# Performance work log

Hardware: AMD Instinct MI355X
Metric: run time of the kernel (lower is better)

## Reference

```python
import math
import jax, jax.numpy as jnp
import numpy as np

B, S, D, H, DH = 2, 2048, 2048, 16, 128  # batch, seq (= n_ctx), d_model, n_heads, d_head


def _alibi_slopes(n):
    def pow2(m):
        start = 2 ** (-2 ** (-(math.log2(m) - 3)))
        return [start * start ** i for i in range(m)]
    if math.log2(n).is_integer():
        return pow2(n)
    c = 2 ** math.floor(math.log2(n))
    return pow2(c) + _alibi_slopes(2 * c)[0::2][: n - c]


def _alibi_mask(n_heads, q_len, kv_len):
    # faithful to _gen_alibi_mask: causal -inf upper triangle + slope * key_position
    slopes = jnp.asarray(np.array(_alibi_slopes(n_heads), dtype=np.float32))  # [H]
    bias = slopes[:, None, None] * jnp.arange(kv_len, dtype=jnp.float32)[None, None, :]  # [H,1,kv]
    i = jnp.arange(q_len)[:, None]
    j = jnp.arange(kv_len)[None, :]
    causal = jnp.where(j > i, -jnp.inf, 0.0).astype(jnp.float32)  # [q,kv] (q_len == kv_len here)
    return causal[None, :, :] + bias  # [H,q,kv]


def setup_inputs() -> dict:
    key = jax.random.key(0)
    k1, k2, k3, k4, k5 = jax.random.split(key, 5)
    scale = 1.0 / math.sqrt(D)
    return {
        "resid_pre": jax.random.normal(k1, (B, S, D), dtype=jnp.float32),
        "Wq": jax.random.normal(k2, (H * DH, D), dtype=jnp.float32) * scale,
        "Wk": jax.random.normal(k3, (H * DH, D), dtype=jnp.float32) * scale,
        "Wv": jax.random.normal(k4, (H * DH, D), dtype=jnp.float32) * scale,
        "Wo": jax.random.normal(k5, (D, H * DH), dtype=jnp.float32) * scale,
    }


def reference(resid_pre, Wq, Wk, Wv, Wo):
    b, s, d = resid_pre.shape
    # nn.Linear(no bias): y = x @ W^T ; view to [b, s, H, DH]
    q = (resid_pre @ Wq.T).reshape(b, s, H, DH)
    k = (resid_pre @ Wk.T).reshape(b, s, H, DH)
    v = (resid_pre @ Wv.T).reshape(b, s, H, DH)
    # QK^T / sqrt(d_head), clamp, add ALiBi+causal mask
    scores = jnp.einsum('bqhd,bkhd->bhqk', q, k) / math.sqrt(DH)
    scores = jnp.clip(scores, -1024.0, 1024.0)
    scores = scores + _alibi_mask(H, s, s)[None]  # broadcast over batch
    attn = jax.nn.softmax(scores.astype(jnp.float32), axis=-1).astype(q.dtype)
    z = jnp.einsum('bhqk,bkhd->bqhd', attn, v)  # [b,s,H,DH]
    # out_proj.weight [D, H*DH] reshaped to [D, H, DH]; per-head out summed over heads
    out = jnp.einsum('bqhd,ohd->bqo', z, Wo.reshape(d, H, DH))
    return out
```

## Files before the change

### kernel.cpp

```cpp
#include <hip/hip_runtime.h>
#include <hip/hip_bf16.h>

typedef __attribute__((ext_vector_type(4))) float f32x4;
typedef __attribute__((ext_vector_type(8))) short bf16x8;
typedef __attribute__((ext_vector_type(4))) short short4v;

__device__ __forceinline__ short f2bf(float f) {
  union { float f; unsigned u; } x; x.f = f;
  unsigned r = x.u + 0x7fffu + ((x.u >> 16) & 1u);
  return (short)(r >> 16);
}

__device__ __forceinline__ float fexp2(float x) {
#if __has_builtin(__builtin_amdgcn_exp2f)
  return __builtin_amdgcn_exp2f(x);
#else
  return exp2f(x);
#endif
}

#define WAITVM(n) { asm volatile("s_waitcnt vmcnt(" #n ")" ::: "memory"); __builtin_amdgcn_sched_barrier(0); }
#define BARRIER() { __builtin_amdgcn_sched_barrier(0); asm volatile("s_barrier" ::: "memory"); __builtin_amdgcn_sched_barrier(0); }
#define GLD16(g, l) __builtin_amdgcn_global_load_lds((const __attribute__((address_space(1))) void*)(g), (__attribute__((address_space(3))) void*)(l), 16, 0, 0)

#define QSC (0.08838834764831845f * 1.4426950408889634f)

__global__ __launch_bounds__(256) void cast_kernel(const float* __restrict__ in,
                                                   short* __restrict__ out, int n4) {
  int i = blockIdx.x * 256 + threadIdx.x;
  if (i < n4) {
    const float4 v = reinterpret_cast<const float4*>(in)[i];
    short4v s;
    s.x = f2bf(v.x); s.y = f2bf(v.y); s.z = f2bf(v.z); s.w = f2bf(v.w);
    reinterpret_cast<short4v*>(out)[i] = s;
  }
}

__global__ __launch_bounds__(256) void cast_w_kernel(const float* __restrict__ w0,
                                                     const float* __restrict__ w1,
                                                     const float* __restrict__ w2,
                                                     const float* __restrict__ w3,
                                                     short* __restrict__ qkv,
                                                     short* __restrict__ wo) {
  const int y = blockIdx.y;
  const float* in = (y == 0) ? w0 : (y == 1) ? w1 : (y == 2) ? w2 : w3;
  short* out = (y < 3) ? (qkv + (long)y * 4194304) : wo;
  const int i = blockIdx.x * 256 + threadIdx.x;
  const float4 v = reinterpret_cast<const float4*>(in)[i];
  short4v s;
  s.x = f2bf(v.x); s.y = f2bf(v.y); s.z = f2bf(v.z); s.w = f2bf(v.w);
  reinterpret_cast<short4v*>(out)[i] = s;
}

__global__ __launch_bounds__(512, 2) void gemm_qkv8(const short* __restrict__ A,
                                                    const short* __restrict__ W,
                                                    short* __restrict__ Qo,
                                                    short* __restrict__ Ko,
                                                    short* __restrict__ Vt) {
  __shared__ __align__(1024) char lds[131072];
  const int tid  = threadIdx.x;
  const int lane = tid & 63;
  const int w    = tid >> 6;
  const int wm   = w >> 2, wn = w & 3;
  const int l16  = lane & 15, g = lane >> 4;
  const int K    = 2048;

  int id = (int)blockIdx.x;
  id = (id & 7) * 64 + (id >> 3);
  const int mb = id & 31, nb = id >> 5;
  const long m0 = (long)mb * 128, n0 = (long)nb * 384;

  const int srow = lane >> 3;
  const int scol = ((lane & 7) ^ srow) * 8;
  const int csw  = (l16 & 7) << 4;

  f32x4 acc[4][6];
  #pragma unroll
  for (int a = 0; a < 4; a++)
    #pragma unroll
    for (int b = 0; b < 6; b++) acc[a][b] = (f32x4){0.f, 0.f, 0.f, 0.f};

  #define STAGE_A(kt, buf)                                                          \
    {                                                                               \
      const short* s0_ = A + (m0 + w * 16 + srow) * K + (kt) * 64 + scol;           \
      char* d_ = lds + (buf) * 65536 + (w * 16) * 128;                              \
      GLD16(s0_, d_);                                                               \
      GLD16(s0_ + 8LL * K, d_ + 1024);                                              \
    }
  #define STAGE_B(h, kt, buf)                                                       \
    {                                                                               \
      const short* s0_ = W + (n0 + (h) * 128 + w * 16 + srow) * K + (kt) * 64 + scol; \
      char* d_ = lds + (buf) * 65536 + 16384 + (h) * 16384 + (w * 16) * 128;        \
      GLD16(s0_, d_);                                                               \
      GLD16(s0_ + 8LL * K, d_ + 1024);                                              \
    }

  #define RDA(buf, fmL, k) (*reinterpret_cast<const bf16x8*>(                       \
      lds + (buf) * 65536 + ((wm * 64 + (fmL) * 16 + l16) * 128) +                  \
      ((((k) * 64 + g * 16)) ^ csw)))
  #define RDB(buf, h, j, k) (*reinterpret_cast<const bf16x8*>(                      \
      lds + (buf) * 65536 + 16384 + (h) * 16384 +                                   \
      ((wn * 16 + (j) * 64 + l16) * 128) + ((((k) * 64 + g * 16)) ^ csw)))

  STAGE_A(0, 0);
  STAGE_B(0, 0, 0);
  STAGE_B(1, 0, 0);
  STAGE_B(2, 0, 0);
  WAITVM(4);
  BARRIER();

  bf16x8 af[4][2], bfr[2][2];
  for (int kt = 0; kt < 32; ++kt) {
    const int cur = kt & 1, nxt = cur ^ 1;
    const int ks = (kt + 1 < 32) ? (kt + 1) : kt;

    #pragma unroll
    for (int fm = 0; fm < 4; fm++)
      #pragma unroll
      for (int k = 0; k < 2; k++) af[fm][k] = RDA(cur, fm, k);
    #pragma unroll
    for (int j = 0; j < 2; j++)
      #pragma unroll
      for (int k = 0; k < 2; k++) bfr[j][k] = RDB(cur, 0, j, k);
    STAGE_A(ks, nxt);
    STAGE_B(0, ks, nxt);
    WAITVM(6);
    BARRIER();
    __builtin_amdgcn_s_setprio(1);
    #pragma unroll
    for (int fm = 0; fm < 4; fm++)
      #pragma unroll
      for (int j = 0; j < 2; j++)
        #pragma unroll
        for (int k = 0; k < 2; k++)
          acc[fm][j] = __builtin_amdgcn_mfma_f32_16x16x32_bf16(af[fm][k], bfr[j][k], acc[fm][j], 0, 0, 0);
    __builtin_amdgcn_s_setprio(0);
    BARRIER();

    #pragma unroll
    for (int j = 0; j < 2; j++)
      #pragma unroll
      for (int k = 0; k < 2; k++) bfr[j][k] = RDB(cur, 1, j, k);
    STAGE_B(1, ks, nxt);
    WAITVM(6);
    BARRIER();
    __builtin_amdgcn_s_setprio(1);
    #pragma unroll
    for (int fm = 0; fm < 4; fm++)
      #pragma unroll
      for (int j = 0; j < 2; j++)
        #pragma unroll
        for (int k = 0; k < 2; k++)
          acc[fm][2 + j] = __builtin_amdgcn_mfma_f32_16x16x32_bf16(af[fm][k], bfr[j][k], acc[fm][2 + j], 0, 0, 0);
    __builtin_amdgcn_s_setprio(0);
    BARRIER();

    #pragma unroll
    for (int j = 0; j < 2; j++)
      #pragma unroll
      for (int k = 0; k < 2; k++) bfr[j][k] = RDB(cur, 2, j, k);
    STAGE_B(2, ks, nxt);
    WAITVM(4);
    BARRIER();
    __builtin_amdgcn_s_setprio(1);
    #pragma unroll
    for (int fm = 0; fm < 4; fm++)
      #pragma unroll
      for (int j = 0; j < 2; j++)
        #pragma unroll
        for (int k = 0; k < 2; k++)
          acc[fm][4 + j] = __builtin_amdgcn_mfma_f32_16x16x32_bf16(af[fm][k], bfr[j][k], acc[fm][4 + j], 0, 0, 0);
    __builtin_amdgcn_s_setprio(0);
    BARRIER();
  }

  #pragma unroll
  for (int fm = 0; fm < 4; fm++)
    #pragma unroll
    for (int fj = 0; fj < 6; fj++) {
      const long row0 = m0 + wm * 64 + fm * 16 + g * 4;
      const long col  = n0 + fj * 64 + wn * 16 + l16;
      if (col < 2048) {
        #pragma unroll
        for (int i = 0; i < 4; i++) Qo[(row0 + i) * 2048 + col] = f2bf(acc[fm][fj][i] * QSC);
      } else if (col < 4096) {
        #pragma unroll
        for (int i = 0; i < 4; i++) Ko[(row0 + i) * 2048 + (col - 2048)] = f2bf(acc[fm][fj][i]);
      } else {
        const long c2 = col - 4096;
        const long base = (((row0 >> 11) * 16 + (c2 >> 7)) * 128 + (c2 & 127)) * 2048 + (row0 & 2047);
        short4v pk;
        #pragma unroll
        for (int i = 0; i < 4; i++) pk[i] = f2bf(acc[fm][fj][i]);
        *reinterpret_cast<short4v*>(Vt + base) = pk;
      }
    }
  #undef STAGE_A
  #undef STAGE_B
  #undef RDA
  #undef RDB
}

__global__ __launch_bounds__(512, 2) void gemm_o2(const short* __restrict__ A,
                                                  const short* __restrict__ W,
                                                  float* __restrict__ C) {
  __shared__ __align__(1024) char lds[98304];
  const int tid  = threadIdx.x;
  const int lane = tid & 63;
  const int w    = tid >> 6;
  const int wm   = w >> 2, wn = w & 3;
  const int l16  = lane & 15, g = lane >> 4;
  const int K    = 2048;

  int id = (int)blockIdx.x;
  id = (id & 7) * 32 + (id >> 3);
  const int mb = id & 31, nb = id >> 5;
  const long m0 = (long)mb * 128, n0 = (long)nb * 256;

  const int srow = lane >> 3;
  const int scol = ((lane & 7) ^ srow) * 8;
  const int csw  = (l16 & 7) << 4;

  f32x4 acc[4][4];
  #pragma unroll
  for (int a = 0; a < 4; a++)
    #pragma unroll
    for (int b = 0; b < 4; b++) acc[a][b] = (f32x4){0.f, 0.f, 0.f, 0.f};

  #define OSTAGE_A(kt, buf)                                                         \
    {                                                                               \
      const short* s0_ = A + (m0 + w * 16 + srow) * K + (kt) * 64 + scol;           \
      char* d_ = lds + (buf) * 49152 + (w * 16) * 128;                              \
      GLD16(s0_, d_);                                                               \
      GLD16(s0_ + 8LL * K, d_ + 1024);                                              \
    }
  #define OSTAGE_B(h, kt, buf)                                                      \
    {                                                                               \
      const short* s0_ = W + (n0 + (h) * 128 + w * 16 + srow) * K + (kt) * 64 + scol; \
      char* d_ = lds + (buf) * 49152 + 16384 + (h) * 16384 + (w * 16) * 128;        \
      GLD16(s0_, d_);                                                               \
      GLD16(s0_ + 8LL * K, d_ + 1024);                                              \
    }
  #define ORDA(buf, fmL, k) (*reinterpret_cast<const bf16x8*>(                      \
      lds + (buf) * 49152 + ((wm * 64 + (fmL) * 16 + l16) * 128) +                  \
      ((((k) * 64 + g * 16)) ^ csw)))
  #define ORDB(buf, h, j, k) (*reinterpret_cast<const bf16x8*>(                     \
      lds + (buf) * 49152 + 16384 + (h) * 16384 +                                   \
      ((wn * 16 + (j) * 64 + l16) * 128) + ((((k) * 64 + g * 16)) ^ csw)))

  OSTAGE_A(0, 0);
  OSTAGE_B(0, 0, 0);
  OSTAGE_B(1, 0, 0);
  WAITVM(2);
  BARRIER();

  bf16x8 af[4][2], bfr[2][2];
  for (int kt = 0; kt < 32; ++kt) {
    const int cur = kt & 1, nxt = cur ^ 1;
    const int ks = (kt + 1 < 32) ? (kt + 1) : kt;

    #pragma unroll
    for (int fm = 0; fm < 4; fm++)
      #pragma unroll
      for (int k = 0; k < 2; k++) af[fm][k] = ORDA(cur, fm, k);
    #pragma unroll
    for (int j = 0; j < 2; j++)
      #pragma unroll
      for (int k = 0; k < 2; k++) bfr[j][k] = ORDB(cur, 0, j, k);
    OSTAGE_A(ks, nxt);
    OSTAGE_B(0, ks, nxt);
    WAITVM(4);
    BARRIER();
    __builtin_amdgcn_s_setprio(1);
    #pragma unroll
    for (int fm = 0; fm < 4; fm++)
      #pragma unroll
      for (int j = 0; j < 2; j++)
        #pragma unroll
        for (int k = 0; k < 2; k++)
          acc[fm][j] = __builtin_amdgcn_mfma_f32_16x16x32_bf16(af[fm][k], bfr[j][k], acc[fm][j], 0, 0, 0);
    __builtin_amdgcn_s_setprio(0);
    BARRIER();

    #pragma unroll
    for (int j = 0; j < 2; j++)
      #pragma unroll
      for (int k = 0; k < 2; k++) bfr[j][k] = ORDB(cur, 1, j, k);
    OSTAGE_B(1, ks, nxt);
    WAITVM(2);
    BARRIER();
    __builtin_amdgcn_s_setprio(1);
    #pragma unroll
    for (int fm = 0; fm < 4; fm++)
      #pragma unroll
      for (int j = 0; j < 2; j++)
        #pragma unroll
        for (int k = 0; k < 2; k++)
          acc[fm][2 + j] = __builtin_amdgcn_mfma_f32_16x16x32_bf16(af[fm][k], bfr[j][k], acc[fm][2 + j], 0, 0, 0);
    __builtin_amdgcn_s_setprio(0);
    BARRIER();
  }

  #pragma unroll
  for (int fm = 0; fm < 4; fm++)
    #pragma unroll
    for (int fn = 0; fn < 4; fn++) {
      const long row0 = m0 + wm * 64 + fm * 16 + g * 4;
      const long col  = n0 + (fn >> 1) * 128 + (fn & 1) * 64 + wn * 16 + l16;
      #pragma unroll
      for (int i = 0; i < 4; i++) C[(row0 + i) * 2048 + col] = acc[fm][fn][i];
    }
  #undef OSTAGE_A
  #undef OSTAGE_B
  #undef ORDA
  #undef ORDB
}

__global__ __launch_bounds__(256, 2) void attn_kernel(const short* __restrict__ Q,
                                                      const short* __restrict__ K,
                                                      const short* __restrict__ Vt,
                                                      short* __restrict__ Z) {
  __shared__ short Ks[64][136];
  __shared__ short Vs[128][72];
  __shared__ short plds[4][32][72];

  const int tid  = threadIdx.x;
  const int lane = tid & 63;
  const int w    = tid >> 6;
  const int l16  = lane & 15, g = lane >> 4;

  const int bh = blockIdx.x;
  const int bx = 15 - (int)blockIdx.y;
  const int b  = bh >> 4, h = bh & 15;
  const int q0 = bx * 128;

  const float LOG2E  = 1.4426950408889634f;
  const float slope2 = exp2f(-0.5f * (float)(h + 1)) * LOG2E;
  const float CLAMP2 = 1477.3197f;

  bf16x8 qf[2][4];
  #pragma unroll
  for (int mi = 0; mi < 2; mi++) {
    const long qoff = ((long)(b * 2048 + q0 + w * 32 + mi * 16 + l16)) * 2048 + h * 128;
    #pragma unroll
    for (int c = 0; c < 4; c++)
      qf[mi][c] = *reinterpret_cast<const bf16x8*>(Q + qoff + c * 32 + g * 8);
  }

  const f32x4 zero4 = {0.f, 0.f, 0.f, 0.f};
  f32x4 zacc[2][8];
  #pragma unroll
  for (int mi = 0; mi < 2; mi++)
    #pragma unroll
    for (int s = 0; s < 8; s++) zacc[mi][s] = zero4;
  float m2[2][4], li[2][4];
  #pragma unroll
  for (int mi = 0; mi < 2; mi++)
    #pragma unroll
    for (int i = 0; i < 4; i++) { m2[mi][i] = -3e38f; li[mi][i] = 0.f; }

  float aj[4];
  #pragma unroll
  for (int ni = 0; ni < 4; ni++) aj[ni] = slope2 * (float)(ni * 16 + l16);

  const int krow = tid >> 4, kcol = (tid & 15) * 8;
  const int vrow = tid >> 3, vcol = (tid & 7) * 8;
  const short* Kh = K + ((long)b * 2048) * 2048 + h * 128;
  const short* Vh = Vt + ((long)(b * 16 + h) * 128) * 2048;

  bf16x8 kreg[4], vreg[4];
  #pragma unroll
  for (int j = 0; j < 4; j++)
    kreg[j] = *reinterpret_cast<const bf16x8*>(Kh + (long)(j * 16 + krow) * 2048 + kcol);
  #pragma unroll
  for (int j = 0; j < 4; j++)
    vreg[j] = *reinterpret_cast<const bf16x8*>(Vh + (long)(j * 32 + vrow) * 2048 + vcol);

  const int ntiles = 2 * bx + 2;
  for (int t = 0; t < ntiles; t++) {
    const int kv0 = t * 64;
    __syncthreads();
    #pragma unroll
    for (int j = 0; j < 4; j++)
      *reinterpret_cast<bf16x8*>(&Ks[j * 16 + krow][kcol]) = kreg[j];
    #pragma unroll
    for (int j = 0; j < 4; j++)
      *reinterpret_cast<bf16x8*>(&Vs[j * 32 + vrow][vcol]) = vreg[j];
    __syncthreads();

    const bool active = (q0 + w * 32 + 31) >= kv0;
    f32x4 sc[2][4];
    if (active) {
      #pragma unroll
      for (int mi = 0; mi < 2; mi++)
        #pragma unroll
        for (int ni = 0; ni < 4; ni++) sc[mi][ni] = zero4;
      #pragma unroll
      for (int ni = 0; ni < 4; ni++)
        #pragma unroll
        for (int kc = 0; kc < 4; kc++) {
          const bf16x8 kf = *reinterpret_cast<const bf16x8*>(&Ks[ni * 16 + l16][kc * 32 + g * 8]);
          #pragma unroll
          for (int mi = 0; mi < 2; mi++)
            sc[mi][ni] = __builtin_amdgcn_mfma_f32_16x16x32_bf16(qf[mi][kc], kf, sc[mi][ni], 0, 0, 0);
        }
    }

    if (t + 1 < ntiles) {
      const short* kb = Kh + (long)(kv0 + 64) * 2048;
      const short* vb = Vh + kv0 + 64;
      #pragma unroll
      for (int j = 0; j < 4; j++)
        kreg[j] = *reinterpret_cast<const bf16x8*>(kb + (long)(j * 16 + krow) * 2048 + kcol);
      #pragma unroll
      for (int j = 0; j < 4; j++)
        vreg[j] = *reinterpret_cast<const bf16x8*>(vb + (long)(j * 32 + vrow) * 2048 + vcol);
    }

    if (active) {
      const float bk = slope2 * (float)kv0;
      float bn[4];
      #pragma unroll
      for (int ni = 0; ni < 4; ni++) bn[ni] = bk + aj[ni];
      float rmax[2][4];
      float slack = -3e38f;
      #pragma unroll
      for (int mi = 0; mi < 2; mi++)
        #pragma unroll
        for (int i = 0; i < 4; i++) {
          const int qi = q0 + w * 32 + mi * 16 + g * 4 + i;
          float mx = -3e38f;
          #pragma unroll
          for (int ni = 0; ni < 4; ni++) {
            const int j = kv0 + ni * 16 + l16;
            float v = fminf(fmaxf(sc[mi][ni][i], -CLAMP2), CLAMP2) + bn[ni];
            v = (j <= qi) ? v : -3e38f;
            sc[mi][ni][i] = v;
            mx = fmaxf(mx, v);
          }
          rmax[mi][i] = mx;
          slack = fmaxf(slack, mx - m2[mi][i]);
        }
      if (__any(slack > 10.f)) {
        #pragma unroll
        for (int mi = 0; mi < 2; mi++)
          #pragma unroll
          for (int i = 0; i < 4; i++) {
            float bb = rmax[mi][i];
            #pragma unroll
            for (int ms = 1; ms < 16; ms <<= 1) bb = fmaxf(bb, __shfl_xor(bb, ms));
            const float mnew = fmaxf(m2[mi][i], bb);
            const float corr = fexp2(m2[mi][i] - mnew);
            m2[mi][i] = mnew;
            li[mi][i] *= corr;
            #pragma unroll
            for (int s = 0; s < 8; s++) zacc[mi][s][i] *= corr;
          }
      }
      #pragma unroll
      for (int mi = 0; mi < 2; mi++)
        #pragma unroll
        for (int i = 0; i < 4; i++) {
          float psum = 0.f;
          #pragma unroll
          for (int ni = 0; ni < 4; ni++) {
            const float p = fexp2(sc[mi][ni][i] - m2[mi][i]);
            plds[w][mi * 16 + g * 4 + i][ni * 16 + l16] = f2bf(p);
            psum += p;
          }
          li[mi][i] += psum;
        }

      bf16x8 paf[2][2];
      #pragma unroll
      for (int mi = 0; mi < 2; mi++)
        #pragma unroll
        for (int kk = 0; kk < 2; kk++)
          paf[mi][kk] = *reinterpret_cast<const bf16x8*>(&plds[w][mi * 16 + l16][kk * 32 + g * 8]);
      #pragma unroll
      for (int s = 0; s < 8; s++) {
        const bf16x8 vf0 = *reinterpret_cast<const bf16x8*>(&Vs[s * 16 + l16][g * 8]);
        const bf16x8 vf1 = *reinterpret_cast<const bf16x8*>(&Vs[s * 16 + l16][32 + g * 8]);
        #pragma unroll
        for (int mi = 0; mi < 2; mi++) {
          zacc[mi][s] = __builtin_amdgcn_mfma_f32_16x16x32_bf16(paf[mi][0], vf0, zacc[mi][s], 0, 0, 0);
          zacc[mi][s] = __builtin_amdgcn_mfma_f32_16x16x32_bf16(paf[mi][1], vf1, zacc[mi][s], 0, 0, 0);
        }
      }
    }
  }

  #pragma unroll
  for (int mi = 0; mi < 2; mi++)
    #pragma unroll
    for (int i = 0; i < 4; i++) {
      float s = li[mi][i];
      #pragma unroll
      for (int ms = 1; ms < 16; ms <<= 1) s += __shfl_xor(s, ms);
      li[mi][i] = s;
    }
  #pragma unroll
  for (int mi = 0; mi < 2; mi++)
    #pragma unroll
    for (int s = 0; s < 8; s++)
      #pragma unroll
      for (int i = 0; i < 4; i++) {
        const int qi = q0 + w * 32 + mi * 16 + g * 4 + i;
        const float zv = zacc[mi][s][i] / li[mi][i];
        Z[((long)(b * 2048 + qi)) * 2048 + h * 128 + s * 16 + l16] = f2bf(zv);
      }
}

extern "C" void kernel_launch(void* const* d_in, const int* in_sizes, int n_in,
                              void* d_out, int out_size, void* d_ws, size_t ws_size,
                              hipStream_t stream) {
  const float* X  = (const float*)d_in[0];
  const float* Wq = (const float*)d_in[1];
  const float* Wk = (const float*)d_in[2];
  const float* Wv = (const float*)d_in[3];
  const float* Wo = (const float*)d_in[4];
  float* out = (float*)d_out;

  short* ws    = (short*)d_ws;
  short* Xb    = ws;
  short* Wqkvb = ws + 8388608;
  short* Wob   = ws + 20971520;
  short* Qb    = ws + 25165824;
  short* Kb    = ws + 33554432;
  short* Vtb   = ws + 41943040;
  short* Zb    = Xb;

  cast_kernel<<<8192, 256, 0, stream>>>(X, Xb, 2097152);
  dim3 gw(4096, 4);
  cast_w_kernel<<<gw, 256, 0, stream>>>(Wq, Wk, Wv, Wo, Wqkvb, Wob);

  gemm_qkv8<<<512, 512, 0, stream>>>(Xb, Wqkvb, Qb, Kb, Vtb);

  dim3 ga(32, 16);
  attn_kernel<<<ga, 256, 0, stream>>>(Qb, Kb, Vtb, Zb);

  gemm_o2<<<256, 512, 0, stream>>>(Zb, Wob, out);
}
```

Before: 263.9 us.

## Shrink attention Q tile to 64 rows, swizzle LDS, raise occupancy

The attention kernel now gives each block 64 query rows (16 per wave) instead of 128 and launches twice as many blocks, which also raises the launch-bounds occupancy hint to 4 blocks per CU. The padded LDS arrays for K, V and P are replaced with unpadded arrays addressed through an XOR swizzle, shrinking shared memory while avoiding bank conflicts. The per-wave causal skip check is removed because every wave now overlaps each tile it visits. The aim is more parallelism and better causal load balance, at the cost of each K/V tile loaded into LDS being reused by half as many query rows, so global K/V traffic roughly doubles.

```diff
diff --git a/kernel.cpp b/kernel.cpp
--- a/kernel.cpp
+++ b/kernel.cpp
@@ -316,13 +316,13 @@
   #undef ORDB
 }
 
-__global__ __launch_bounds__(256, 2) void attn_kernel(const short* __restrict__ Q,
+__global__ __launch_bounds__(256, 4) void attn_kernel(const short* __restrict__ Q,
                                                       const short* __restrict__ K,
                                                       const short* __restrict__ Vt,
                                                       short* __restrict__ Z) {
-  __shared__ short Ks[64][136];
-  __shared__ short Vs[128][72];
-  __shared__ short plds[4][32][72];
+  __shared__ short Ks[64][128];
+  __shared__ short Vs[128][64];
+  __shared__ short plds[4][16][64];
 
   const int tid  = threadIdx.x;
   const int lane = tid & 63;
@@ -330,34 +330,28 @@
   const int l16  = lane & 15, g = lane >> 4;
 
   const int bh = blockIdx.x;
-  const int bx = 15 - (int)blockIdx.y;
+  const int bx = 31 - (int)blockIdx.y;
   const int b  = bh >> 4, h = bh & 15;
-  const int q0 = bx * 128;
-
-  const float LOG2E  = 1.4426950408889634f;
-  const float slope2 = exp2f(-0.5f * (float)(h + 1)) * LOG2E;
+  const int q0 = bx * 64;
+
+  const float slope2 = exp2f(-0.5f * (float)(h + 1)) * 1.4426950408889634f;
   const float CLAMP2 = 1477.3197f;
 
-  bf16x8 qf[2][4];
-  #pragma unroll
-  for (int mi = 0; mi < 2; mi++) {
-    const long qoff = ((long)(b * 2048 + q0 + w * 32 + mi * 16 + l16)) * 2048 + h * 128;
+  bf16x8 qf[4];
+  {
+    const long qoff = ((long)(b * 2048 + q0 + w * 16 + l16)) * 2048 + h * 128;
     #pragma unroll
     for (int c = 0; c < 4; c++)
-      qf[mi][c] = *reinterpret_cast<const bf16x8*>(Q + qoff + c * 32 + g * 8);
+      qf[c] = *reinterpret_cast<const bf16x8*>(Q + qoff + c * 32 + g * 8);
   }
 
   const f32x4 zero4 = {0.f, 0.f, 0.f, 0.f};
-  f32x4 zacc[2][8];
-  #pragma unroll
-  for (int mi = 0; mi < 2; mi++)
-    #pragma unroll
-    for (int s = 0; s < 8; s++) zacc[mi][s] = zero4;
-  float m2[2][4], li[2][4];
-  #pragma unroll
-  for (int mi = 0; mi < 2; mi++)
-    #pragma unroll
-    for (int i = 0; i < 4; i++) { m2[mi][i] = -3e38f; li[mi][i] = 0.f; }
+  f32x4 zacc[8];
+  #pragma unroll
+  for (int s = 0; s < 8; s++) zacc[s] = zero4;
+  float m2[4], li[4];
+  #pragma unroll
+  for (int i = 0; i < 4; i++) { m2[i] = -3e38f; li[i] = 0.f; }
 
   float aj[4];
   #pragma unroll
@@ -365,6 +359,10 @@
 
   const int krow = tid >> 4, kcol = (tid & 15) * 8;
   const int vrow = tid >> 3, vcol = (tid & 7) * 8;
+  const int kswz = (krow & 7) << 5;
+  const int vswz = (vrow & 7) << 4;
+  const int rswz = (l16 & 7) << 4;
+  const int kr5  = (l16 & 7) << 5;
   const short* Kh = K + ((long)b * 2048) * 2048 + h * 128;
   const short* Vh = Vt + ((long)(b * 16 + h) * 128) * 2048;
 
@@ -376,35 +374,31 @@
   for (int j = 0; j < 4; j++)
     vreg[j] = *reinterpret_cast<const bf16x8*>(Vh + (long)(j * 32 + vrow) * 2048 + vcol);
 
-  const int ntiles = 2 * bx + 2;
+  const int ntiles = bx + 1;
   for (int t = 0; t < ntiles; t++) {
     const int kv0 = t * 64;
     __syncthreads();
     #pragma unroll
     for (int j = 0; j < 4; j++)
-      *reinterpret_cast<bf16x8*>(&Ks[j * 16 + krow][kcol]) = kreg[j];
+      *reinterpret_cast<bf16x8*>(reinterpret_cast<char*>(Ks) +
+          (j * 16 + krow) * 256 + ((kcol * 2) ^ kswz)) = kreg[j];
     #pragma unroll
     for (int j = 0; j < 4; j++)
-      *reinterpret_cast<bf16x8*>(&Vs[j * 32 + vrow][vcol]) = vreg[j];
+      *reinterpret_cast<bf16x8*>(reinterpret_cast<char*>(Vs) +
+          (j * 32 + vrow) * 128 + ((vcol * 2) ^ vswz)) = vreg[j];
     __syncthreads();
 
-    const bool active = (q0 + w * 32 + 31) >= kv0;
-    f32x4 sc[2][4];
-    if (active) {
-      #pragma unroll
-      for (int mi = 0; mi < 2; mi++)
-        #pragma unroll
-        for (int ni = 0; ni < 4; ni++) sc[mi][ni] = zero4;
-      #pragma unroll
-      for (int ni = 0; ni < 4; ni++)
-        #pragma unroll
-        for (int kc = 0; kc < 4; kc++) {
-          const bf16x8 kf = *reinterpret_cast<const bf16x8*>(&Ks[ni * 16 + l16][kc * 32 + g * 8]);
-          #pragma unroll
-          for (int mi = 0; mi < 2; mi++)
-            sc[mi][ni] = __builtin_amdgcn_mfma_f32_16x16x32_bf16(qf[mi][kc], kf, sc[mi][ni], 0, 0, 0);
-        }
-    }
+    f32x4 sc[4];
+    #pragma unroll
+    for (int ni = 0; ni < 4; ni++) sc[ni] = zero4;
+    #pragma unroll
+    for (int ni = 0; ni < 4; ni++)
+      #pragma unroll
+      for (int kc = 0; kc < 4; kc++) {
+        const bf16x8 kf = *reinterpret_cast<const bf16x8*>(
+            reinterpret_cast<const char*>(Ks) + (ni * 16 + l16) * 256 + ((kc * 64 + g * 16) ^ kr5));
+        sc[ni] = __builtin_amdgcn_mfma_f32_16x16x32_bf16(qf[kc], kf, sc[ni], 0, 0, 0);
+      }
 
     if (t + 1 < ntiles) {
       const short* kb = Kh + (long)(kv0 + 64) * 2048;
@@ -417,98 +411,86 @@
         vreg[j] = *reinterpret_cast<const bf16x8*>(vb + (long)(j * 32 + vrow) * 2048 + vcol);
     }
 
-    if (active) {
-      const float bk = slope2 * (float)kv0;
-      float bn[4];
-      #pragma unroll
-      for (int ni = 0; ni < 4; ni++) bn[ni] = bk + aj[ni];
-      float rmax[2][4];
-      float slack = -3e38f;
-      #pragma unroll
-      for (int mi = 0; mi < 2; mi++)
-        #pragma unroll
-        for (int i = 0; i < 4; i++) {
-          const int qi = q0 + w * 32 + mi * 16 + g * 4 + i;
-          float mx = -3e38f;
-          #pragma unroll
-          for (int ni = 0; ni < 4; ni++) {
-            const int j = kv0 + ni * 16 + l16;
-            float v = fminf(fmaxf(sc[mi][ni][i], -CLAMP2), CLAMP2) + bn[ni];
-            v = (j <= qi) ? v : -3e38f;
-            sc[mi][ni][i] = v;
-            mx = fmaxf(mx, v);
-          }
-          rmax[mi][i] = mx;
-          slack = fmaxf(slack, mx - m2[mi][i]);
-        }
-      if (__any(slack > 10.f)) {
-        #pragma unroll
-        for (int mi = 0; mi < 2; mi++)
-          #pragma unroll
-          for (int i = 0; i < 4; i++) {
-            float bb = rmax[mi][i];
-            #pragma unroll
-            for (int ms = 1; ms < 16; ms <<= 1) bb = fmaxf(bb, __shfl_xor(bb, ms));
-            const float mnew = fmaxf(m2[mi][i], bb);
-            const float corr = fexp2(m2[mi][i] - mnew);
-            m2[mi][i] = mnew;
-            li[mi][i] *= corr;
-            #pragma unroll
-            for (int s = 0; s < 8; s++) zacc[mi][s][i] *= corr;
-          }
+    const float bk = slope2 * (float)kv0;
+    float bn[4];
+    #pragma unroll
+    for (int ni = 0; ni < 4; ni++) bn[ni] = bk + aj[ni];
+    float rmax[4];
+    float slack = -3e38f;
+    #pragma unroll
+    for (int i = 0; i < 4; i++) {
+      const int qi = q0 + w * 16 + g * 4 + i;
+      float mx = -3e38f;
+      #pragma unroll
+      for (int ni = 0; ni < 4; ni++) {
+        const int j = kv0 + ni * 16 + l16;
+        float v = fminf(fmaxf(sc[ni][i], -CLAMP2), CLAMP2) + bn[ni];
+        v = (j <= qi) ? v : -3e38f;
+        sc[ni][i] = v;
+        mx = fmaxf(mx, v);
       }
-      #pragma unroll
-      for (int mi = 0; mi < 2; mi++)
-        #pragma unroll
-        for (int i = 0; i < 4; i++) {
-          float psum = 0.f;
-          #pragma unroll
-          for (int ni = 0; ni < 4; ni++) {
-            const float p = fexp2(sc[mi][ni][i] - m2[mi][i]);
-            plds[w][mi * 16 + g * 4 + i][ni * 16 + l16] = f2bf(p);
-            psum += p;
-          }
-          li[mi][i] += psum;
-        }
-
-      bf16x8 paf[2][2];
-      #pragma unroll
-      for (int mi = 0; mi < 2; mi++)
-        #pragma unroll
-        for (int kk = 0; kk < 2; kk++)
-          paf[mi][kk] = *reinterpret_cast<const bf16x8*>(&plds[w][mi * 16 + l16][kk * 32 + g * 8]);
-      #pragma unroll
-      for (int s = 0; s < 8; s++) {
-        const bf16x8 vf0 = *reinterpret_cast<const bf16x8*>(&Vs[s * 16 + l16][g * 8]);
-        const bf16x8 vf1 = *reinterpret_cast<const bf16x8*>(&Vs[s * 16 + l16][32 + g * 8]);
-        #pragma unroll
-        for (int mi = 0; mi < 2; mi++) {
-          zacc[mi][s] = __builtin_amdgcn_mfma_f32_16x16x32_bf16(paf[mi][0], vf0, zacc[mi][s], 0, 0, 0);
-          zacc[mi][s] = __builtin_amdgcn_mfma_f32_16x16x32_bf16(paf[mi][1], vf1, zacc[mi][s], 0, 0, 0);
-        }
+      rmax[i] = mx;
+      slack = fmaxf(slack, mx - m2[i]);
+    }
+    if (__any(slack > 10.f)) {
+      #pragma unroll
+      for (int i = 0; i < 4; i++) {
+        float bb = rmax[i];
+        #pragma unroll
+        for (int ms = 1; ms < 16; ms <<= 1) bb = fmaxf(bb, __shfl_xor(bb, ms));
+        const float mnew = fmaxf(m2[i], bb);
+        const float corr = fexp2(m2[i] - mnew);
+        m2[i] = mnew;
+        li[i] *= corr;
+        #pragma unroll
+        for (int s = 0; s < 8; s++) zacc[s][i] *= corr;
       }
     }
+    char* pbase = reinterpret_cast<char*>(plds) + w * 2048;
+    #pragma unroll
+    for (int i = 0; i < 4; i++) {
+      const int prow = g * 4 + i;
+      const int pswz = (prow & 7) << 4;
+      float psum = 0.f;
+      #pragma unroll
+      for (int ni = 0; ni < 4; ni++) {
+        const float p = fexp2(sc[ni][i] - m2[i]);
+        *reinterpret_cast<short*>(pbase + prow * 128 + (((ni * 16 + l16) * 2) ^ pswz)) = f2bf(p);
+        psum += p;
+      }
+      li[i] += psum;
+    }
+
+    bf16x8 paf[2];
+    #pragma unroll
+    for (int kk = 0; kk < 2; kk++)
+      paf[kk] = *reinterpret_cast<const bf16x8*>(
+          pbase + l16 * 128 + ((kk * 64 + g * 16) ^ rswz));
+    #pragma unroll
+    for (int s = 0; s < 8; s++) {
+      const char* vr = reinterpret_cast<const char*>(Vs) + (s * 16 + l16) * 128;
+      const bf16x8 vf0 = *reinterpret_cast<const bf16x8*>(vr + ((g * 16) ^ rswz));
+      const bf16x8 vf1 = *reinterpret_cast<const bf16x8*>(vr + ((64 + g * 16) ^ rswz));
+      zacc[s] = __builtin_amdgcn_mfma_f32_16x16x32_bf16(paf[0], vf0, zacc[s], 0, 0, 0);
+      zacc[s] = __builtin_amdgcn_mfma_f32_16x16x32_bf16(paf[1], vf1, zacc[s], 0, 0, 0);
+    }
   }
 
   #pragma unroll
-  for (int mi = 0; mi < 2; mi++)
+  for (int i = 0; i < 4; i++) {
+    float s = li[i];
+    #pragma unroll
+    for (int ms = 1; ms < 16; ms <<= 1) s += __shfl_xor(s, ms);
+    li[i] = s;
+  }
+  #pragma unroll
+  for (int s = 0; s < 8; s++)
     #pragma unroll
     for (int i = 0; i < 4; i++) {
-      float s = li[mi][i];
-      #pragma unroll
-      for (int ms = 1; ms < 16; ms <<= 1) s += __shfl_xor(s, ms);
-      li[mi][i] = s;
-    }
-  #pragma unroll
-  for (int mi = 0; mi < 2; mi++)
-    #pragma unroll
-    for (int s = 0; s < 8; s++)
-      #pragma unroll
-      for (int i = 0; i < 4; i++) {
-        const int qi = q0 + w * 32 + mi * 16 + g * 4 + i;
-        const float zv = zacc[mi][s][i] / li[mi][i];
-        Z[((long)(b * 2048 + qi)) * 2048 + h * 128 + s * 16 + l16] = f2bf(zv);
-      }
+      const int qi = q0 + w * 16 + g * 4 + i;
+      const float zv = zacc[s][i] / li[i];
+      Z[((long)(b * 2048 + qi)) * 2048 + h * 128 + s * 16 + l16] = f2bf(zv);
+    }
 }
 
 extern "C" void kernel_launch(void* const* d_in, const int* in_sizes, int n_in,
@@ -536,7 +518,7 @@
 
   gemm_qkv8<<<512, 512, 0, stream>>>(Xb, Wqkvb, Qb, Kb, Vtb);
 
-  dim3 ga(32, 16);
+  dim3 ga(32, 32);
   attn_kernel<<<ga, 256, 0, stream>>>(Qb, Kb, Vtb, Zb);
 
   gemm_o2<<<256, 512, 0, stream>>>(Zb, Wob, out);
```

Measured after the change: 365.8 us. +38.6%, slower.
